# Optimization experiments

Measured on AMD Instinct MI355X. Metric: run time of the kernel, lower is better.

## Reference

```python
import jax, jax.numpy as jnp
import numpy as np

B, T, D, H, TE = 4, 8192, 512, 8, 2048
Dh = D // H
EPS = 1e-5


def layer_norm(x, g, b):
    mu = jnp.mean(x, axis=-1, keepdims=True)
    var = jnp.mean(jnp.square(x - mu), axis=-1, keepdims=True)
    return (x - mu) * jax.lax.rsqrt(var + EPS) * g + b


def setup_inputs() -> dict:
    key = jax.random.key(0)
    ks = jax.random.split(key, 8)
    s = 0.02  # typical init scale
    return {
        "x": jax.random.normal(ks[0], (B, T, D), jnp.float32),
        "emb": jax.random.normal(ks[1], (B, TE), jnp.float32),
        "src_mask": (jax.random.uniform(ks[2], (B, T, 1)) > 0.2).astype(jnp.float32),
        "gamma": jnp.ones((D,), jnp.float32),
        "beta": jnp.zeros((D,), jnp.float32),
        "Wq": jax.random.normal(ks[3], (D, D), jnp.float32) * s,
        "bq": jnp.zeros((D,), jnp.float32),
        "Wk": jax.random.normal(ks[4], (D, D), jnp.float32) * s,
        "bk": jnp.zeros((D,), jnp.float32),
        "Wv": jax.random.normal(ks[5], (D, D), jnp.float32) * s,
        "bv": jnp.zeros((D,), jnp.float32),
        "emb_W": jax.random.normal(ks[6], (TE, 2 * D), jnp.float32) * s,
        "emb_b": jnp.zeros((2 * D,), jnp.float32),
        "gamma2": jnp.ones((D,), jnp.float32),
        "beta2": jnp.zeros((D,), jnp.float32),
        "out_W": jax.random.normal(ks[7], (D, D), jnp.float32) * s,
        "out_b": jnp.zeros((D,), jnp.float32),
    }


def reference(x, emb, src_mask, gamma, beta, Wq, bq, Wk, bk, Wv, bv,
              emb_W, emb_b, gamma2, beta2, out_W, out_b):
    # x: (B,T,D); emb: (B,TE); src_mask: (B,T,1)
    xn = layer_norm(x, gamma, beta)  # single LN reused (same math as 3 calls)
    q = xn @ Wq + bq
    k = xn @ Wk + bk + (1.0 - src_mask) * -1000000.0
    v = (xn @ Wv + bv) * src_mask
    q = jax.nn.softmax(q.reshape(B, T, H, Dh), axis=-1)  # softmax over head dim
    k = jax.nn.softmax(k.reshape(B, T, H, Dh), axis=1)   # softmax over time
    v = v.reshape(B, T, H, Dh)
    attn = jnp.einsum('bthd,bthl->bhdl', k, v)           # (B,H,Dh,Dh) KV state
    y = jnp.einsum('bthd,bhdl->bthl', q, attn).reshape(B, T, D)
    # StylizationBlock (dropout inactive in eval)
    emb_out = jax.nn.silu(emb) @ emb_W + emb_b           # (B, 2D)
    scale, shift = jnp.split(emb_out[:, None, :], 2, axis=2)
    h = layer_norm(y, gamma2, beta2) * (1.0 + scale) + shift
    h = jax.nn.silu(h) @ out_W + out_b
    return x + h
```

## Files before the change

kernel.cpp:

```cpp
#include <hip/hip_runtime.h>
#include <cstdint>
#include <cstddef>

typedef unsigned short u16;
typedef unsigned int u32;
typedef __attribute__((ext_vector_type(8))) short short8;
typedef __attribute__((ext_vector_type(4))) float f32x4;

static constexpr int CB = 4;
static constexpr int CT = 8192;
static constexpr int CD = 512;
static constexpr int CH = 8;
static constexpr int CDH = 64;
static constexpr int CTE = 2048;
static constexpr int CD2 = 1024;

__device__ __forceinline__ float b2f(u16 u) {
    return __uint_as_float(((u32)u) << 16);
}
__device__ __forceinline__ u16 f2b(float f) {
    u32 i = __float_as_uint(f);
    i = i + 0x7fffu + ((i >> 16) & 1u);
    return (u16)(i >> 16);
}

typedef const __attribute__((address_space(1))) void* gas_p;
typedef __attribute__((address_space(3))) void* las_p;
#define GLD16(g, l) __builtin_amdgcn_global_load_lds((gas_p)(g), (las_p)(l), 16, 0, 0)

__global__ __launch_bounds__(256) void zero_kernel(float* __restrict__ p, int n) {
    int i = blockIdx.x * 256 + threadIdx.x;
    if (i < n) p[i] = 0.0f;
}

__global__ __launch_bounds__(256) void wconv_kernel(
        const float* __restrict__ W0, const float* __restrict__ W1,
        const float* __restrict__ W2, const float* __restrict__ W3,
        u16* __restrict__ Wt)
{
    const float* W;
    switch (blockIdx.y) {
        case 0: W = W0; break;
        case 1: W = W1; break;
        case 2: W = W2; break;
        default: W = W3; break;
    }
    u16* o = Wt + (size_t)blockIdx.y * CD * CD;
    const int k0 = (blockIdx.x >> 3) * 64;
    const int n0 = (blockIdx.x & 7) * 64;
    const int tid = threadIdx.x;
    __shared__ u16 tile[64][65];
    const int nn = tid & 63, kq = tid >> 6;
#pragma unroll
    for (int i = 0; i < 16; i++) {
        const int kk = i * 4 + kq;
        tile[kk][nn] = f2b(W[(size_t)(k0 + kk) * CD + n0 + nn]);
    }
    __syncthreads();
    const int kk2 = tid & 63, nq = tid >> 6;
#pragma unroll
    for (int i = 0; i < 16; i++) {
        const int nn2 = i * 4 + nq;
        o[(size_t)(n0 + nn2) * CD + k0 + kk2] = tile[kk2][nn2];
    }
}

__global__ __launch_bounds__(256) void ln1_kernel(const float* __restrict__ x,
        const float* __restrict__ g, const float* __restrict__ bt,
        u16* __restrict__ xn)
{
    const int row = blockIdx.x;
    const int tid = threadIdx.x;
    const float2 p = ((const float2*)(x + (size_t)row * CD))[tid];
    float s = p.x + p.y;
    float sq = p.x * p.x + p.y * p.y;
#pragma unroll
    for (int m = 1; m < 64; m <<= 1) { s += __shfl_xor(s, m); sq += __shfl_xor(sq, m); }
    __shared__ float red[8];
    const int wid = tid >> 6;
    if ((tid & 63) == 0) { red[wid] = s; red[wid + 4] = sq; }
    __syncthreads();
    s = red[0] + red[1] + red[2] + red[3];
    sq = red[4] + red[5] + red[6] + red[7];
    const float mu = s * (1.0f / CD);
    float var = sq * (1.0f / CD) - mu * mu;
    var = fmaxf(var, 0.0f);
    const float rs = rsqrtf(var + 1e-5f);
    const float2 gv = ((const float2*)g)[tid];
    const float2 bv = ((const float2*)bt)[tid];
    const float y0 = (p.x - mu) * rs * gv.x + bv.x;
    const float y1 = (p.y - mu) * rs * gv.y + bv.y;
    ((u32*)(xn + (size_t)row * CD))[tid] = (u32)f2b(y0) | ((u32)f2b(y1) << 16);
}

__global__ __launch_bounds__(256) void gemm_mfma(
    const u16* __restrict__ A, const u16* __restrict__ Bt,
    const float* __restrict__ bias, const float* __restrict__ bias2,
    void* __restrict__ Cv, void* __restrict__ Cv2,
    const float* __restrict__ mask, const float* __restrict__ xres,
    int mode)
{
    __shared__ u16 As[2][128][32];
    __shared__ u16 Bs[2][128][32];
    const int tid = threadIdx.x;
    const int wave = tid >> 6, lane = tid & 63;
    const int quad = lane >> 4, l16 = lane & 15;

    const int n = blockIdx.x;
    const int xcd = n & 7;
    int by, bx;
    if (mode == 4) { const int slot = n >> 3; by = xcd * 32 + (slot >> 3); bx = slot & 7; }
    else           { const int slot = n >> 3; by = xcd * 32 + (slot >> 2); bx = slot & 3; }
    const int row0 = by * 128;
    const int col0 = bx * 128;
    const int wm = (wave >> 1) * 64, wn = (wave & 1) * 64;

    int emode = mode;
    const float* bptr = bias;
    void* cout = Cv;
    int ocol0 = col0;
    if (mode == 4) {
        if (col0 >= 512) { emode = 2; bptr = bias2; cout = Cv2; ocol0 = col0 - 512; }
        else emode = 1;
    }

    f32x4 acc[4][4];
#pragma unroll
    for (int mt = 0; mt < 4; mt++)
#pragma unroll
        for (int nt = 0; nt < 4; nt++)
            acc[mt][nt] = (f32x4){0.0f, 0.0f, 0.0f, 0.0f};

    const int srow = lane >> 2;
    const int sslot = lane & 3;
    const int swz = (srow >> 1) & 3;
    const int aw0 = wave * 16;
    const u16* gA0 = A + (size_t)(row0 + aw0 + srow) * CD + (sslot ^ swz) * 8;
    const u16* gA1 = gA0 + (size_t)64 * CD;
    const u16* gB0 = Bt + (size_t)(col0 + aw0 + srow) * CD + (sslot ^ swz) * 8;
    const u16* gB1 = gB0 + (size_t)64 * CD;

#define STAGE_T(bf, kt) do { \
        GLD16(gA0 + (kt) * 32, &As[bf][aw0][0]); \
        GLD16(gA1 + (kt) * 32, &As[bf][aw0 + 64][0]); \
        GLD16(gB0 + (kt) * 32, &Bs[bf][aw0][0]); \
        GLD16(gB1 + (kt) * 32, &Bs[bf][aw0 + 64][0]); \
    } while (0)

    STAGE_T(0, 0);

    const int swsel = (quad ^ ((l16 >> 1) & 3)) * 8;

#pragma unroll
    for (int t = 0; t < 16; ++t) {
        const int bf = t & 1;
        if (t < 15) STAGE_T(bf ^ 1, t + 1);
        if (t < 15) asm volatile("s_waitcnt vmcnt(4)\ns_barrier" ::: "memory");
        else        asm volatile("s_waitcnt vmcnt(0)\ns_barrier" ::: "memory");

        short8 af[4], bfr[4];
#pragma unroll
        for (int mt = 0; mt < 4; mt++)
            af[mt] = *(const short8*)&As[bf][wm + mt * 16 + l16][swsel];
#pragma unroll
        for (int nt = 0; nt < 4; nt++)
            bfr[nt] = *(const short8*)&Bs[bf][wn + nt * 16 + l16][swsel];
        __builtin_amdgcn_s_setprio(1);
#pragma unroll
        for (int mt = 0; mt < 4; mt++)
#pragma unroll
            for (int nt = 0; nt < 4; nt++)
                acc[mt][nt] = __builtin_amdgcn_mfma_f32_16x16x32_bf16(
                    af[mt], bfr[nt], acc[mt][nt], 0, 0, 0);
        __builtin_amdgcn_s_setprio(0);
        asm volatile("s_waitcnt lgkmcnt(0)\ns_barrier" ::: "memory");
    }
#undef STAGE_T

    if (emode == 3) {
#pragma unroll
        for (int mt = 0; mt < 4; mt++) {
            const int rbase = row0 + wm + mt * 16 + quad * 4;
#pragma unroll
            for (int r = 0; r < 4; r++) {
                const int row = rbase + r;
#pragma unroll
                for (int nt = 0; nt < 4; nt++) {
                    const int col = ocol0 + wn + nt * 16 + l16;
                    const float val = acc[mt][nt][r] + bptr[col];
                    ((float*)cout)[(size_t)row * CD + col] =
                        val + xres[(size_t)row * CD + col];
                }
            }
        }
    } else {
        float* stg = (wave < 2 ? (float*)&As[0][0][0] : (float*)&Bs[0][0][0])
                   + (wave & 1) * (16 * 65);
#pragma unroll
        for (int mt = 0; mt < 4; mt++) {
#pragma unroll
            for (int r = 0; r < 4; r++) {
                const int rr = quad * 4 + r;
                const int grow = row0 + wm + mt * 16 + rr;
                float mval = 0.0f;
                if (emode == 1 || emode == 2) mval = mask[grow];
#pragma unroll
                for (int nt = 0; nt < 4; nt++) {
                    const int ocol = ocol0 + wn + nt * 16 + l16;
                    float val = acc[mt][nt][r] + bptr[ocol];
                    if (emode == 1) val += (1.0f - mval) * -1000000.0f;
                    else if (emode == 2) val *= mval;
                    stg[rr * 65 + nt * 16 + l16] = val;
                }
            }
            u16* cbase = (u16*)cout + (size_t)(row0 + wm + mt * 16) * CD + ocol0 + wn;
#pragma unroll
            for (int i = 0; i < 8; i++) {
                const int rr = i * 2 + (lane >> 5);
                const int c2 = lane & 31;
                const float f0 = stg[rr * 65 + 2 * c2];
                const float f1 = stg[rr * 65 + 2 * c2 + 1];
                ((u32*)(cbase + (size_t)rr * CD))[c2] =
                    (u32)f2b(f0) | ((u32)f2b(f1) << 16);
            }
        }
    }
}

__global__ __launch_bounds__(256) void ksm_partial(const u16* __restrict__ k,
        float* __restrict__ pm, float* __restrict__ ps)
{
    const int bid = blockIdx.x;
    const int b = bid >> 5, ch = bid & 31;
    const int tid = threadIdx.x;
    const u32* base = (const u32*)(k + (size_t)b * CT * CD + (size_t)ch * 256 * CD) + tid;
    float m0 = -3.0e38f, m1 = -3.0e38f;
#pragma unroll 8
    for (int r = 0; r < 256; ++r) {
        const u32 p = base[(size_t)r * 256];
        m0 = fmaxf(m0, b2f((u16)(p & 0xffff)));
        m1 = fmaxf(m1, b2f((u16)(p >> 16)));
    }
    float s0 = 0.0f, s1 = 0.0f;
#pragma unroll 8
    for (int r = 0; r < 256; ++r) {
        const u32 p = base[(size_t)r * 256];
        s0 += __expf(b2f((u16)(p & 0xffff)) - m0);
        s1 += __expf(b2f((u16)(p >> 16)) - m1);
    }
    const int d0 = tid * 2;
    pm[((size_t)b * CD + d0) * 32 + ch] = m0;
    pm[((size_t)b * CD + d0 + 1) * 32 + ch] = m1;
    ps[((size_t)b * CD + d0) * 32 + ch] = s0;
    ps[((size_t)b * CD + d0 + 1) * 32 + ch] = s1;
}

__global__ __launch_bounds__(256) void ksm_norm(u16* __restrict__ k,
        const float* __restrict__ pm, const float* __restrict__ ps)
{
    const int bid = blockIdx.x;
    const int b = bid >> 5, ch = bid & 31;
    const int tid = threadIdx.x;
    const int d0 = tid * 2;
    const float* pm0 = pm + ((size_t)b * CD + d0) * 32;
    const float* pm1 = pm0 + 32;
    const float* ps0 = ps + ((size_t)b * CD + d0) * 32;
    const float* ps1 = ps0 + 32;
    float M0 = -3.0e38f, M1 = -3.0e38f;
#pragma unroll
    for (int c = 0; c < 32; ++c) { M0 = fmaxf(M0, pm0[c]); M1 = fmaxf(M1, pm1[c]); }
    float S0 = 0.0f, S1 = 0.0f;
#pragma unroll
    for (int c = 0; c < 32; ++c) {
        S0 += ps0[c] * __expf(pm0[c] - M0);
        S1 += ps1[c] * __expf(pm1[c] - M1);
    }
    const float R0 = 1.0f / S0, R1 = 1.0f / S1;
    u32* base = (u32*)(k + (size_t)b * CT * CD + (size_t)ch * 256 * CD) + tid;
#pragma unroll 4
    for (int r = 0; r < 256; ++r) {
        const u32 p = base[(size_t)r * 256];
        const float x0 = __expf(b2f((u16)(p & 0xffff)) - M0) * R0;
        const float x1 = __expf(b2f((u16)(p >> 16)) - M1) * R1;
        base[(size_t)r * 256] = (u32)f2b(x0) | ((u32)f2b(x1) << 16);
    }
}

__global__ __launch_bounds__(256) void attn_kernel(const u16* __restrict__ k,
        const u16* __restrict__ v, float* __restrict__ attn)
{
    const int bid = blockIdx.x;
    const int bh = bid >> 4, ch = bid & 15;
    const int b = bh >> 3, h = bh & 7;
    const int tid = threadIdx.x;
    __shared__ u16 Ks[32][64], Vs[32][64];
    const int ti = tid >> 4, tj = tid & 15;
    const int d0 = ti * 4, l0 = tj * 4;
    const int trow = tid >> 3, cg8 = (tid & 7) * 8;
    float acc[4][4];
#pragma unroll
    for (int r = 0; r < 4; r++)
#pragma unroll
        for (int c = 0; c < 4; c++) acc[r][c] = 0.0f;

    for (int st = 0; st < 16; st++) {
        const int t0 = ch * 512 + st * 32;
        const size_t goff = ((size_t)(b * CT + t0 + trow)) * CD + h * 64 + cg8;
        const uint4 kv4 = *(const uint4*)(k + goff);
        const uint4 vv4 = *(const uint4*)(v + goff);
        __syncthreads();
        *(uint4*)&Ks[trow][cg8] = kv4;
        *(uint4*)&Vs[trow][cg8] = vv4;
        __syncthreads();
#pragma unroll
        for (int tt = 0; tt < 32; tt++) {
            const ushort4 ka = *(const ushort4*)&Ks[tt][d0];
            const ushort4 va = *(const ushort4*)&Vs[tt][l0];
            const float kr[4] = { b2f(ka.x), b2f(ka.y), b2f(ka.z), b2f(ka.w) };
            const float vr[4] = { b2f(va.x), b2f(va.y), b2f(va.z), b2f(va.w) };
#pragma unroll
            for (int r = 0; r < 4; r++)
#pragma unroll
                for (int c = 0; c < 4; c++)
                    acc[r][c] = fmaf(kr[r], vr[c], acc[r][c]);
        }
    }
    float* ab = attn + (size_t)bh * 64 * 64;
#pragma unroll
    for (int r = 0; r < 4; r++)
#pragma unroll
        for (int c = 0; c < 4; c++)
            atomicAdd(&ab[(d0 + r) * 64 + l0 + c], acc[r][c]);
}

__global__ __launch_bounds__(256) void y_mfma(const u16* __restrict__ q,
        const float* __restrict__ attn, u16* __restrict__ y)
{
    const int bid = blockIdx.x;
    const int bh = bid >> 5;
    const int chunk = bid & 31;
    const int b = bh >> 3, h = bh & 7;
    const int tid = threadIdx.x;
    const int wave = tid >> 6, lane = tid & 63;
    const int quad = lane >> 4, l16 = lane & 15;

    __shared__ u16 Bh[64][72];
    __shared__ u16 Bl[64][72];
    __shared__ float Ys[4][16][65];

    const float* ab = attn + (size_t)bh * 64 * 64;
#pragma unroll
    for (int i = 0; i < 16; i++) {
        const int idx = i * 256 + tid;
        const int d = idx >> 6, l = idx & 63;
        const float a = ab[idx];
        const u16 hi = f2b(a);
        Bh[l][d] = hi;
        Bl[l][d] = f2b(a - b2f(hi));
    }
    __syncthreads();

    short8 bhf[4][2], blf[4][2];
#pragma unroll
    for (int nt = 0; nt < 4; nt++)
#pragma unroll
        for (int ks = 0; ks < 2; ks++) {
            bhf[nt][ks] = *(const short8*)&Bh[nt * 16 + l16][ks * 32 + quad * 8];
            blf[nt][ks] = *(const short8*)&Bl[nt * 16 + l16][ks * 32 + quad * 8];
        }

    const int rowbase = chunk * 256 + wave * 64;
    const size_t qb = ((size_t)(b * CT + rowbase)) * CD + h * 64;

#pragma unroll
    for (int it = 0; it < 4; it++) {
        const u16* qp = q + qb + (size_t)(it * 16 + l16) * CD + quad * 8;
        const uint4 q0 = *(const uint4*)qp;
        const uint4 q1 = *(const uint4*)(qp + 32);
        float xv[16];
        const u32 qw[8] = { q0.x, q0.y, q0.z, q0.w, q1.x, q1.y, q1.z, q1.w };
#pragma unroll
        for (int j = 0; j < 8; j++) {
            xv[2 * j]     = b2f((u16)(qw[j] & 0xffff));
            xv[2 * j + 1] = b2f((u16)(qw[j] >> 16));
        }
        float m = xv[0];
#pragma unroll
        for (int j = 1; j < 16; j++) m = fmaxf(m, xv[j]);
        m = fmaxf(m, __shfl_xor(m, 16));
        m = fmaxf(m, __shfl_xor(m, 32));
        float s = 0.0f;
#pragma unroll
        for (int j = 0; j < 16; j++) { xv[j] = __expf(xv[j] - m); s += xv[j]; }
        s += __shfl_xor(s, 16);
        s += __shfl_xor(s, 32);
        const float rinv = 1.0f / s;
        short8 ah[2], al[2];
#pragma unroll
        for (int ks = 0; ks < 2; ks++)
#pragma unroll
            for (int j = 0; j < 8; j++) {
                const float v = xv[ks * 8 + j] * rinv;
                const u16 hi = f2b(v);
                ah[ks][j] = (short)hi;
                al[ks][j] = (short)f2b(v - b2f(hi));
            }

        f32x4 acc[4];
#pragma unroll
        for (int nt = 0; nt < 4; nt++) acc[nt] = (f32x4){0.f, 0.f, 0.f, 0.f};
#pragma unroll
        for (int nt = 0; nt < 4; nt++) {
            acc[nt] = __builtin_amdgcn_mfma_f32_16x16x32_bf16(ah[0], bhf[nt][0], acc[nt], 0, 0, 0);
            acc[nt] = __builtin_amdgcn_mfma_f32_16x16x32_bf16(ah[1], bhf[nt][1], acc[nt], 0, 0, 0);
            acc[nt] = __builtin_amdgcn_mfma_f32_16x16x32_bf16(ah[0], blf[nt][0], acc[nt], 0, 0, 0);
            acc[nt] = __builtin_amdgcn_mfma_f32_16x16x32_bf16(ah[1], blf[nt][1], acc[nt], 0, 0, 0);
            acc[nt] = __builtin_amdgcn_mfma_f32_16x16x32_bf16(al[0], bhf[nt][0], acc[nt], 0, 0, 0);
            acc[nt] = __builtin_amdgcn_mfma_f32_16x16x32_bf16(al[1], bhf[nt][1], acc[nt], 0, 0, 0);
        }

#pragma unroll
        for (int nt = 0; nt < 4; nt++)
#pragma unroll
            for (int rr = 0; rr < 4; rr++)
                Ys[wave][quad * 4 + rr][nt * 16 + l16] = acc[nt][rr];
        u32* yo = (u32*)y + ((size_t)(b * CT + rowbase + it * 16)) * (CD / 2) + h * 32;
#pragma unroll
        for (int p = 0; p < 8; p++) {
            const int idx = p * 64 + lane;
            const int row = idx >> 5, c2 = idx & 31;
            const float f0 = Ys[wave][row][2 * c2];
            const float f1 = Ys[wave][row][2 * c2 + 1];
            yo[(size_t)row * (CD / 2) + c2] = (u32)f2b(f0) | ((u32)f2b(f1) << 16);
        }
    }
}

__global__ __launch_bounds__(256) void embsilu_kernel(const float* __restrict__ emb,
        float* __restrict__ se)
{
    const int i = blockIdx.x * 256 + threadIdx.x;
    if (i < CB * CTE) {
        const float e = emb[i];
        se[i] = e / (1.0f + __expf(-e));
    }
}
__global__ __launch_bounds__(256) void eoinit_kernel(const float* __restrict__ embB,
        float* __restrict__ eo)
{
    const int i = blockIdx.x * 256 + threadIdx.x;
    if (i < CB * CD2) eo[i] = embB[i & (CD2 - 1)];
}
__global__ __launch_bounds__(256) void embout2_kernel(const float* __restrict__ se,
        const float* __restrict__ embW, float* __restrict__ eo)
{
    const int jg = blockIdx.x & 15, kc = blockIdx.x >> 4;
    const int tid = threadIdx.x;
    const int jl = tid & 63, kgrp = tid >> 6;
    const int j = jg * 64 + jl;
    const int kbase = kc * 256 + kgrp * 64;
    const float* W = embW + (size_t)kbase * CD2 + j;
    const float* s0 = se + kbase;
    const float* s1 = s0 + CTE;
    const float* s2 = s1 + CTE;
    const float* s3 = s2 + CTE;
    float a0 = 0.0f, a1 = 0.0f, a2 = 0.0f, a3 = 0.0f;
#pragma unroll 8
    for (int kk = 0; kk < 64; kk++) {
        const float w = W[(size_t)kk * CD2];
        a0 = fmaf(s0[kk], w, a0);
        a1 = fmaf(s1[kk], w, a1);
        a2 = fmaf(s2[kk], w, a2);
        a3 = fmaf(s3[kk], w, a3);
    }
    __shared__ float red[4][4][64];
    red[kgrp][0][jl] = a0; red[kgrp][1][jl] = a1;
    red[kgrp][2][jl] = a2; red[kgrp][3][jl] = a3;
    __syncthreads();
    if (tid < 64) {
#pragma unroll
        for (int b = 0; b < 4; b++) {
            const float t = red[0][b][tid] + red[1][b][tid]
                          + red[2][b][tid] + red[3][b][tid];
            atomicAdd(&eo[(size_t)b * CD2 + jg * 64 + tid], t);
        }
    }
}

__global__ __launch_bounds__(256) void ln2_style_kernel(const u16* __restrict__ y,
        const float* __restrict__ g2, const float* __restrict__ bt2,
        const float* __restrict__ eo, u16* __restrict__ sout)
{
    const int row = blockIdx.x;
    const int tid = threadIdx.x;
    const int b = row >> 13;
    const u32 p = ((const u32*)(y + (size_t)row * CD))[tid];
    const float x0 = b2f((u16)(p & 0xffff));
    const float x1 = b2f((u16)(p >> 16));
    float s = x0 + x1;
    float sq = x0 * x0 + x1 * x1;
#pragma unroll
    for (int m = 1; m < 64; m <<= 1) { s += __shfl_xor(s, m); sq += __shfl_xor(sq, m); }
    __shared__ float red[8];
    const int wid = tid >> 6;
    if ((tid & 63) == 0) { red[wid] = s; red[wid + 4] = sq; }
    __syncthreads();
    s = red[0] + red[1] + red[2] + red[3];
    sq = red[4] + red[5] + red[6] + red[7];
    const float mu = s * (1.0f / CD);
    float var = sq * (1.0f / CD) - mu * mu;
    var = fmaxf(var, 0.0f);
    const float rs = rsqrtf(var + 1e-5f);
    const float2 gv = ((const float2*)g2)[tid];
    const float2 bv = ((const float2*)bt2)[tid];
    const float2 sc = ((const float2*)(eo + (size_t)b * CD2))[tid];
    const float2 sh = ((const float2*)(eo + (size_t)b * CD2 + CD))[tid];
    float h0 = (x0 - mu) * rs * gv.x + bv.x;
    float h1 = (x1 - mu) * rs * gv.y + bv.y;
    h0 = h0 * (1.0f + sc.x) + sh.x;
    h1 = h1 * (1.0f + sc.y) + sh.y;
    const float s0 = h0 / (1.0f + __expf(-h0));
    const float s1 = h1 / (1.0f + __expf(-h1));
    ((u32*)(sout + (size_t)row * CD))[tid] = (u32)f2b(s0) | ((u32)f2b(s1) << 16);
}

extern "C" void kernel_launch(void* const* d_in, const int* in_sizes, int n_in,
                              void* d_out, int out_size, void* d_ws, size_t ws_size,
                              hipStream_t stream) {
    (void)in_sizes; (void)n_in; (void)out_size; (void)ws_size;
    const float* x    = (const float*)d_in[0];
    const float* emb  = (const float*)d_in[1];
    const float* mask = (const float*)d_in[2];
    const float* gamma= (const float*)d_in[3];
    const float* beta = (const float*)d_in[4];
    const float* Wq   = (const float*)d_in[5];
    const float* bq   = (const float*)d_in[6];
    const float* Wk   = (const float*)d_in[7];
    const float* bk   = (const float*)d_in[8];
    const float* Wv   = (const float*)d_in[9];
    const float* bv   = (const float*)d_in[10];
    const float* embW = (const float*)d_in[11];
    const float* embB = (const float*)d_in[12];
    const float* g2   = (const float*)d_in[13];
    const float* bt2  = (const float*)d_in[14];
    const float* outW = (const float*)d_in[15];
    const float* outb = (const float*)d_in[16];

    char* od = (char*)d_out;
    u16* kq  = (u16*)od;
    u16* vy  = (u16*)(od + 33554432);
    float* outp = (float*)d_out;

    char* ws = (char*)d_ws;
    u16* xn   = (u16*)ws;
    u16* WtK  = (u16*)(ws + 33554432);
    u16* WtV  = WtK + (size_t)CD * CD;
    u16* WtQ  = WtV + (size_t)CD * CD;
    u16* WtO  = WtQ + (size_t)CD * CD;
    float* pm   = (float*)(ws + 35651584);
    float* ps   = (float*)(ws + 35651584 + 262144);
    float* attn = (float*)(ws + 35651584);
    float* eo   = (float*)(ws + 36306944);
    float* se   = (float*)(ws + 36323328);

    wconv_kernel<<<dim3(64, 4), 256, 0, stream>>>(Wk, Wv, Wq, outW, WtK);
    ln1_kernel<<<CB * CT, 256, 0, stream>>>(x, gamma, beta, xn);
    embsilu_kernel<<<32, 256, 0, stream>>>(emb, se);
    eoinit_kernel<<<16, 256, 0, stream>>>(embB, eo);
    embout2_kernel<<<128, 256, 0, stream>>>(se, embW, eo);
    gemm_mfma<<<2048, 256, 0, stream>>>(xn, WtK, bk, bv, kq, vy, mask, nullptr, 4);
    ksm_partial<<<128, 256, 0, stream>>>(kq, pm, ps);
    ksm_norm<<<128, 256, 0, stream>>>(kq, pm, ps);
    zero_kernel<<<512, 256, 0, stream>>>(attn, CB * CH * CDH * CDH);
    attn_kernel<<<512, 256, 0, stream>>>(kq, vy, attn);
    gemm_mfma<<<1024, 256, 0, stream>>>(xn, WtQ, bq, nullptr, kq, nullptr, nullptr, nullptr, 0);
    y_mfma<<<1024, 256, 0, stream>>>(kq, attn, vy);
    ln2_style_kernel<<<CB * CT, 256, 0, stream>>>(vy, g2, bt2, eo, xn );
    gemm_mfma<<<1024, 256, 0, stream>>>(xn , WtO, outb, nullptr, outp, nullptr, nullptr, x, 3);
}
```

Baseline: 471.9 us.

## Enlarge GEMM tiles to 256x256 with 512-thread blocks

Changes the bf16 MFMA GEMM from 128x128 tiles on 256 threads to 256x256 tiles on 512 threads (8 waves, each computing 128x64). A and B share one LDS buffer, the grid shrinks by four, and the XCD-aware block mapping is updated to match. The goal is higher arithmetic intensity per LDS/global load and fewer blocks. In exchange each thread holds twice as many accumulator registers, occupancy drops (launch_bounds 512,1), and with only 256 blocks for the 512-column GEMMs, wave-level parallelism across CUs is reduced.

```diff
diff --git a/kernel.cpp b/kernel.cpp
--- a/kernel.cpp
+++ b/kernel.cpp
@@ -93,15 +93,14 @@
     ((u32*)(xn + (size_t)row * CD))[tid] = (u32)f2b(y0) | ((u32)f2b(y1) << 16);
 }
 
-__global__ __launch_bounds__(256) void gemm_mfma(
+__global__ __launch_bounds__(512, 1) void gemm_mfma(
     const u16* __restrict__ A, const u16* __restrict__ Bt,
     const float* __restrict__ bias, const float* __restrict__ bias2,
     void* __restrict__ Cv, void* __restrict__ Cv2,
     const float* __restrict__ mask, const float* __restrict__ xres,
     int mode)
 {
-    __shared__ u16 As[2][128][32];
-    __shared__ u16 Bs[2][128][32];
+    __shared__ u16 SH[2][512][32];
     const int tid = threadIdx.x;
     const int wave = tid >> 6, lane = tid & 63;
     const int quad = lane >> 4, l16 = lane & 15;
@@ -109,11 +108,12 @@
     const int n = blockIdx.x;
     const int xcd = n & 7;
     int by, bx;
-    if (mode == 4) { const int slot = n >> 3; by = xcd * 32 + (slot >> 3); bx = slot & 7; }
-    else           { const int slot = n >> 3; by = xcd * 32 + (slot >> 2); bx = slot & 3; }
-    const int row0 = by * 128;
-    const int col0 = bx * 128;
-    const int wm = (wave >> 1) * 64, wn = (wave & 1) * 64;
+    if (mode == 4) { const int slot = n >> 3; by = xcd * 16 + (slot >> 2); bx = slot & 3; }
+    else           { const int slot = n >> 3; by = xcd * 16 + (slot >> 1); bx = slot & 1; }
+    const int row0 = by * 256;
+    const int col0 = bx * 256;
+    const int wm = (wave >> 2) * 128;
+    const int wn = (wave & 3) * 64;
 
     int emode = mode;
     const float* bptr = bias;
@@ -124,9 +124,9 @@
         else emode = 1;
     }
 
-    f32x4 acc[4][4];
-#pragma unroll
-    for (int mt = 0; mt < 4; mt++)
+    f32x4 acc[8][4];
+#pragma unroll
+    for (int mt = 0; mt < 8; mt++)
 #pragma unroll
         for (int nt = 0; nt < 4; nt++)
             acc[mt][nt] = (f32x4){0.0f, 0.0f, 0.0f, 0.0f};
@@ -134,17 +134,17 @@
     const int srow = lane >> 2;
     const int sslot = lane & 3;
     const int swz = (srow >> 1) & 3;
-    const int aw0 = wave * 16;
+    const int aw0 = wave * 32;
     const u16* gA0 = A + (size_t)(row0 + aw0 + srow) * CD + (sslot ^ swz) * 8;
-    const u16* gA1 = gA0 + (size_t)64 * CD;
+    const u16* gA1 = gA0 + (size_t)16 * CD;
     const u16* gB0 = Bt + (size_t)(col0 + aw0 + srow) * CD + (sslot ^ swz) * 8;
-    const u16* gB1 = gB0 + (size_t)64 * CD;
+    const u16* gB1 = gB0 + (size_t)16 * CD;
 
 #define STAGE_T(bf, kt) do { \
-        GLD16(gA0 + (kt) * 32, &As[bf][aw0][0]); \
-        GLD16(gA1 + (kt) * 32, &As[bf][aw0 + 64][0]); \
-        GLD16(gB0 + (kt) * 32, &Bs[bf][aw0][0]); \
-        GLD16(gB1 + (kt) * 32, &Bs[bf][aw0 + 64][0]); \
+        GLD16(gA0 + (kt) * 32, &SH[bf][aw0][0]); \
+        GLD16(gA1 + (kt) * 32, &SH[bf][aw0 + 16][0]); \
+        GLD16(gB0 + (kt) * 32, &SH[bf][256 + aw0][0]); \
+        GLD16(gB1 + (kt) * 32, &SH[bf][256 + aw0 + 16][0]); \
     } while (0)
 
     STAGE_T(0, 0);
@@ -158,20 +158,19 @@
         if (t < 15) asm volatile("s_waitcnt vmcnt(4)\ns_barrier" ::: "memory");
         else        asm volatile("s_waitcnt vmcnt(0)\ns_barrier" ::: "memory");
 
-        short8 af[4], bfr[4];
-#pragma unroll
-        for (int mt = 0; mt < 4; mt++)
-            af[mt] = *(const short8*)&As[bf][wm + mt * 16 + l16][swsel];
+        short8 bfr[4];
 #pragma unroll
         for (int nt = 0; nt < 4; nt++)
-            bfr[nt] = *(const short8*)&Bs[bf][wn + nt * 16 + l16][swsel];
+            bfr[nt] = *(const short8*)&SH[bf][256 + wn + nt * 16 + l16][swsel];
         __builtin_amdgcn_s_setprio(1);
 #pragma unroll
-        for (int mt = 0; mt < 4; mt++)
+        for (int mt = 0; mt < 8; mt++) {
+            const short8 af = *(const short8*)&SH[bf][wm + mt * 16 + l16][swsel];
 #pragma unroll
             for (int nt = 0; nt < 4; nt++)
                 acc[mt][nt] = __builtin_amdgcn_mfma_f32_16x16x32_bf16(
-                    af[mt], bfr[nt], acc[mt][nt], 0, 0, 0);
+                    af, bfr[nt], acc[mt][nt], 0, 0, 0);
+        }
         __builtin_amdgcn_s_setprio(0);
         asm volatile("s_waitcnt lgkmcnt(0)\ns_barrier" ::: "memory");
     }
@@ -179,7 +178,7 @@
 
     if (emode == 3) {
 #pragma unroll
-        for (int mt = 0; mt < 4; mt++) {
+        for (int mt = 0; mt < 8; mt++) {
             const int rbase = row0 + wm + mt * 16 + quad * 4;
 #pragma unroll
             for (int r = 0; r < 4; r++) {
@@ -194,10 +193,9 @@
             }
         }
     } else {
-        float* stg = (wave < 2 ? (float*)&As[0][0][0] : (float*)&Bs[0][0][0])
-                   + (wave & 1) * (16 * 65);
-#pragma unroll
-        for (int mt = 0; mt < 4; mt++) {
+        float* stg = ((float*)&SH[0][0][0]) + wave * 1040;
+#pragma unroll
+        for (int mt = 0; mt < 8; mt++) {
 #pragma unroll
             for (int r = 0; r < 4; r++) {
                 const int rr = quad * 4 + r;
@@ -568,13 +566,13 @@
     embsilu_kernel<<<32, 256, 0, stream>>>(emb, se);
     eoinit_kernel<<<16, 256, 0, stream>>>(embB, eo);
     embout2_kernel<<<128, 256, 0, stream>>>(se, embW, eo);
-    gemm_mfma<<<2048, 256, 0, stream>>>(xn, WtK, bk, bv, kq, vy, mask, nullptr, 4);
+    gemm_mfma<<<512, 512, 0, stream>>>(xn, WtK, bk, bv, kq, vy, mask, nullptr, 4);
     ksm_partial<<<128, 256, 0, stream>>>(kq, pm, ps);
     ksm_norm<<<128, 256, 0, stream>>>(kq, pm, ps);
     zero_kernel<<<512, 256, 0, stream>>>(attn, CB * CH * CDH * CDH);
     attn_kernel<<<512, 256, 0, stream>>>(kq, vy, attn);
-    gemm_mfma<<<1024, 256, 0, stream>>>(xn, WtQ, bq, nullptr, kq, nullptr, nullptr, nullptr, 0);
+    gemm_mfma<<<256, 512, 0, stream>>>(xn, WtQ, bq, nullptr, kq, nullptr, nullptr, nullptr, 0);
     y_mfma<<<1024, 256, 0, stream>>>(kq, attn, vy);
     ln2_style_kernel<<<CB * CT, 256, 0, stream>>>(vy, g2, bt2, eo, xn );
-    gemm_mfma<<<1024, 256, 0, stream>>>(xn , WtO, outb, nullptr, outp, nullptr, nullptr, x, 3);
-}
+    gemm_mfma<<<256, 512, 0, stream>>>(xn , WtO, outb, nullptr, outp, nullptr, nullptr, x, 3);
+}
```

After: 452.2 us. 4.2% less time.
